# Performance work log

Hardware: AMD Instinct MI355X
Metric: run time of the kernel (lower is better)

## Reference

```python
import jax, jax.numpy as jnp
import numpy as np

S, B, C, H, W = 4, 8, 9, 512, 512

def setup_inputs() -> dict:
    key = jax.random.key(0)
    k1, k2 = jax.random.split(key)
    predictions = jax.random.normal(k1, (S, B, C, H, W), dtype=jnp.float32)
    w = jax.random.normal(k2, (S, C), dtype=jnp.float32) * 0.1  # 1x1 conv weights per stage
    b = jnp.zeros((S,), dtype=jnp.float32)                      # 1x1 conv biases per stage
    return {"predictions": predictions, "w": w, "b": b}

def reference(predictions, w, b):
    # per-stage 1x1 conv (C -> 1): [S,B,H,W]
    wm = jnp.einsum('sbchw,sc->sbhw', predictions, w) + b[:, None, None, None]
    # softmax over stage dim S
    weights = jax.nn.softmax(wm, axis=0)  # [S,B,H,W]
    # weighted sum over stages -> [B,C,H,W]
    fused = jnp.einsum('sbhw,sbchw->bchw', weights, predictions)
    return fused
```

## Files before the change

### kernel.cpp

```cpp
#include <hip/hip_runtime.h>
#include <math.h>

constexpr int  Sn = 4;
constexpr int  Bn = 8;
constexpr int  Cn = 9;
constexpr int  HWc = 512 * 512;
constexpr long SSTRIDE = (long)Bn * Cn * HWc;

__device__ __forceinline__ float4 f4(float v) { return make_float4(v, v, v, v); }

__global__ __launch_bounds__(256) void weighted_fusion_kernel(
    const float* __restrict__ pred,
    const float* __restrict__ wmat,
    const float* __restrict__ bvec,
    float* __restrict__ out)
{
    int tid = blockIdx.x * 256 + threadIdx.x;
    long p4 = (long)tid * 4;
    int b  = (int)(p4 >> 18);
    int hw = (int)(p4 & (HWc - 1));

    const float* tbase = pred + (long)b * Cn * HWc + hw;

    float4 acc[Cn];
    float4 m, l;
    {
        float4 pr[Cn];
        float4 wm = f4(bvec[0]);
        #pragma unroll
        for (int c = 0; c < Cn; ++c) {
            pr[c] = *reinterpret_cast<const float4*>(tbase + (long)c * HWc);
            float wc = wmat[c];
            wm.x += pr[c].x * wc; wm.y += pr[c].y * wc;
            wm.z += pr[c].z * wc; wm.w += pr[c].w * wc;
        }
        m = wm;
        l = f4(1.0f);
        #pragma unroll
        for (int c = 0; c < Cn; ++c) acc[c] = pr[c];
    }

    #pragma unroll
    for (int s = 1; s < Sn; ++s) {
        float4 pr[Cn];
        float4 wm = f4(bvec[s]);
        #pragma unroll
        for (int c = 0; c < Cn; ++c) {
            pr[c] = *reinterpret_cast<const float4*>(tbase + (long)s * SSTRIDE + (long)c * HWc);
            float wc = wmat[s * Cn + c];
            wm.x += pr[c].x * wc; wm.y += pr[c].y * wc;
            wm.z += pr[c].z * wc; wm.w += pr[c].w * wc;
        }
        float4 nm;
        nm.x = fmaxf(m.x, wm.x); nm.y = fmaxf(m.y, wm.y);
        nm.z = fmaxf(m.z, wm.z); nm.w = fmaxf(m.w, wm.w);
        float4 alpha, pw;
        alpha.x = __expf(m.x - nm.x); alpha.y = __expf(m.y - nm.y);
        alpha.z = __expf(m.z - nm.z); alpha.w = __expf(m.w - nm.w);
        pw.x = __expf(wm.x - nm.x); pw.y = __expf(wm.y - nm.y);
        pw.z = __expf(wm.z - nm.z); pw.w = __expf(wm.w - nm.w);
        l.x = l.x * alpha.x + pw.x; l.y = l.y * alpha.y + pw.y;
        l.z = l.z * alpha.z + pw.z; l.w = l.w * alpha.w + pw.w;
        #pragma unroll
        for (int c = 0; c < Cn; ++c) {
            acc[c].x = acc[c].x * alpha.x + pw.x * pr[c].x;
            acc[c].y = acc[c].y * alpha.y + pw.y * pr[c].y;
            acc[c].z = acc[c].z * alpha.z + pw.z * pr[c].z;
            acc[c].w = acc[c].w * alpha.w + pw.w * pr[c].w;
        }
        m = nm;
    }

    float4 rl;
    rl.x = 1.0f / l.x; rl.y = 1.0f / l.y; rl.z = 1.0f / l.z; rl.w = 1.0f / l.w;
    float* obase = out + (long)b * Cn * HWc + hw;
    #pragma unroll
    for (int c = 0; c < Cn; ++c) {
        float4 o;
        o.x = acc[c].x * rl.x; o.y = acc[c].y * rl.y;
        o.z = acc[c].z * rl.z; o.w = acc[c].w * rl.w;
        *reinterpret_cast<float4*>(obase + (long)c * HWc) = o;
    }
}

extern "C" void kernel_launch(void* const* d_in, const int* in_sizes, int n_in,
                              void* d_out, int out_size, void* d_ws, size_t ws_size,
                              hipStream_t stream) {
    const float* pred = (const float*)d_in[0];
    const float* w    = (const float*)d_in[1];
    const float* bias = (const float*)d_in[2];
    float* out        = (float*)d_out;

    const int total_threads = (Bn * HWc) / 4;
    const int block = 256;
    const int grid  = total_threads / block;
    weighted_fusion_kernel<<<grid, block, 0, stream>>>(pred, w, bias, out);
}
```

Before: 417.8 us.

## Issue all stage loads up front with nontemporal hints and two-pass softmax

```diff
diff --git a/kernel.cpp b/kernel.cpp
--- a/kernel.cpp
+++ b/kernel.cpp
@@ -7,7 +7,7 @@
 constexpr int  HWc = 512 * 512;
 constexpr long SSTRIDE = (long)Bn * Cn * HWc;
 
-__device__ __forceinline__ float4 f4(float v) { return make_float4(v, v, v, v); }
+typedef float v4f __attribute__((ext_vector_type(4)));
 
 __global__ __launch_bounds__(256) void weighted_fusion_kernel(
     const float* __restrict__ pred,
@@ -22,64 +22,55 @@
 
     const float* tbase = pred + (long)b * Cn * HWc + hw;
 
-    float4 acc[Cn];
-    float4 m, l;
-    {
-        float4 pr[Cn];
-        float4 wm = f4(bvec[0]);
+    v4f pr[Sn][Cn];
+    #pragma unroll
+    for (int s = 0; s < Sn; ++s) {
         #pragma unroll
         for (int c = 0; c < Cn; ++c) {
-            pr[c] = *reinterpret_cast<const float4*>(tbase + (long)c * HWc);
-            float wc = wmat[c];
-            wm.x += pr[c].x * wc; wm.y += pr[c].y * wc;
-            wm.z += pr[c].z * wc; wm.w += pr[c].w * wc;
+            const v4f* p = reinterpret_cast<const v4f*>(
+                tbase + (long)s * SSTRIDE + (long)c * HWc);
+            pr[s][c] = __builtin_nontemporal_load(p);
         }
-        m = wm;
-        l = f4(1.0f);
-        #pragma unroll
-        for (int c = 0; c < Cn; ++c) acc[c] = pr[c];
     }
 
+    v4f wm[Sn];
+    #pragma unroll
+    for (int s = 0; s < Sn; ++s) {
+        v4f a = bvec[s];
+        #pragma unroll
+        for (int c = 0; c < Cn; ++c) {
+            float wc = wmat[s * Cn + c];
+            a += pr[s][c] * wc;
+        }
+        wm[s] = a;
+    }
+
+    v4f m = wm[0];
     #pragma unroll
     for (int s = 1; s < Sn; ++s) {
-        float4 pr[Cn];
-        float4 wm = f4(bvec[s]);
-        #pragma unroll
-        for (int c = 0; c < Cn; ++c) {
-            pr[c] = *reinterpret_cast<const float4*>(tbase + (long)s * SSTRIDE + (long)c * HWc);
-            float wc = wmat[s * Cn + c];
-            wm.x += pr[c].x * wc; wm.y += pr[c].y * wc;
-            wm.z += pr[c].z * wc; wm.w += pr[c].w * wc;
-        }
-        float4 nm;
-        nm.x = fmaxf(m.x, wm.x); nm.y = fmaxf(m.y, wm.y);
-        nm.z = fmaxf(m.z, wm.z); nm.w = fmaxf(m.w, wm.w);
-        float4 alpha, pw;
-        alpha.x = __expf(m.x - nm.x); alpha.y = __expf(m.y - nm.y);
-        alpha.z = __expf(m.z - nm.z); alpha.w = __expf(m.w - nm.w);
-        pw.x = __expf(wm.x - nm.x); pw.y = __expf(wm.y - nm.y);
-        pw.z = __expf(wm.z - nm.z); pw.w = __expf(wm.w - nm.w);
-        l.x = l.x * alpha.x + pw.x; l.y = l.y * alpha.y + pw.y;
-        l.z = l.z * alpha.z + pw.z; l.w = l.w * alpha.w + pw.w;
-        #pragma unroll
-        for (int c = 0; c < Cn; ++c) {
-            acc[c].x = acc[c].x * alpha.x + pw.x * pr[c].x;
-            acc[c].y = acc[c].y * alpha.y + pw.y * pr[c].y;
-            acc[c].z = acc[c].z * alpha.z + pw.z * pr[c].z;
-            acc[c].w = acc[c].w * alpha.w + pw.w * pr[c].w;
-        }
-        m = nm;
+        m.x = fmaxf(m.x, wm[s].x); m.y = fmaxf(m.y, wm[s].y);
+        m.z = fmaxf(m.z, wm[s].z); m.w = fmaxf(m.w, wm[s].w);
     }
+    v4f p[Sn];
+    v4f l = 0.0f;
+    #pragma unroll
+    for (int s = 0; s < Sn; ++s) {
+        p[s].x = __expf(wm[s].x - m.x); p[s].y = __expf(wm[s].y - m.y);
+        p[s].z = __expf(wm[s].z - m.z); p[s].w = __expf(wm[s].w - m.w);
+        l += p[s];
+    }
+    v4f rl;
+    rl.x = 1.0f / l.x; rl.y = 1.0f / l.y; rl.z = 1.0f / l.z; rl.w = 1.0f / l.w;
+    #pragma unroll
+    for (int s = 0; s < Sn; ++s) p[s] *= rl;
 
-    float4 rl;
-    rl.x = 1.0f / l.x; rl.y = 1.0f / l.y; rl.z = 1.0f / l.z; rl.w = 1.0f / l.w;
     float* obase = out + (long)b * Cn * HWc + hw;
     #pragma unroll
     for (int c = 0; c < Cn; ++c) {
-        float4 o;
-        o.x = acc[c].x * rl.x; o.y = acc[c].y * rl.y;
-        o.z = acc[c].z * rl.z; o.w = acc[c].w * rl.w;
-        *reinterpret_cast<float4*>(obase + (long)c * HWc) = o;
+        v4f o = p[0] * pr[0][c];
+        #pragma unroll
+        for (int s = 1; s < Sn; ++s) o += p[s] * pr[s][c];
+        __builtin_nontemporal_store(o, reinterpret_cast<v4f*>(obase + (long)c * HWc));
     }
 }
 
```

After: 396.0 us. 5.2% less time.
